# Kernel tuning notes

Measured on AMD Instinct MI355X. Metric: run time of the kernel, lower is better.

Reference implementation:

```python
import jax, jax.numpy as jnp
import numpy as np

N, E = 50000, 400000
IN, HID, HEADS, OUT, EDIM = 128, 16, 8, 128, 32


def _lin(key, fan_in, fan_out, bias=True):
    k1, k2 = jax.random.split(key)
    s = 1.0 / np.sqrt(fan_in)
    W = jax.random.uniform(k1, (fan_in, fan_out), jnp.float32, -s, s)
    if bias:
        b = jax.random.uniform(k2, (fan_out,), jnp.float32, -s, s)
        return W, b
    return W


def setup_inputs() -> dict:
    key = jax.random.key(0)
    ks = jax.random.split(key, 16)
    x = jax.random.normal(ks[0], (N, IN), jnp.float32)
    edge_index = jax.random.randint(ks[1], (2, E), 0, N, jnp.int64)
    edge_feats = jax.random.normal(ks[2], (E, EDIM), jnp.float32)
    H1 = HEADS * HID  # 128
    Wq1, bq1 = _lin(ks[3], IN, H1)
    Wk1, bk1 = _lin(ks[4], IN, H1)
    Wv1, bv1 = _lin(ks[5], IN, H1)
    We1 = _lin(ks[6], EDIM, H1, bias=False)
    Ws1, bs1 = _lin(ks[7], IN, H1)
    Wq2, bq2 = _lin(ks[8], H1, OUT)
    Wk2, bk2 = _lin(ks[9], H1, OUT)
    Wv2, bv2 = _lin(ks[10], H1, OUT)
    We2 = _lin(ks[11], EDIM, OUT, bias=False)
    Ws2, bs2 = _lin(ks[12], H1, OUT)
    return dict(x=x, edge_index=edge_index, edge_feats=edge_feats,
                Wq1=Wq1, bq1=bq1, Wk1=Wk1, bk1=bk1, Wv1=Wv1, bv1=bv1, We1=We1, Ws1=Ws1, bs1=bs1,
                Wq2=Wq2, bq2=bq2, Wk2=Wk2, bk2=bk2, Wv2=Wv2, bv2=bv2, We2=We2, Ws2=Ws2, bs2=bs2)


def transformer_conv(x, src, dst, e, Wq, bq, Wk, bk, Wv, bv, We, Ws, bs, heads, ch, concat):
    # PyG TransformerConv: project at nodes, gather to edges.
    n = x.shape[0]
    q = (x @ Wq + bq).reshape(n, heads, ch)[dst]          # [E,H,C]
    k = (x @ Wk + bk).reshape(n, heads, ch)[src]
    v = (x @ Wv + bv).reshape(n, heads, ch)[src]
    ee = (e @ We).reshape(-1, heads, ch)                   # edge conditioning
    k = k + ee
    v = v + ee
    alpha = (q * k).sum(-1) / jnp.sqrt(jnp.asarray(ch, x.dtype))  # [E,H]
    # per-destination segment softmax
    m = jax.ops.segment_max(alpha, dst, num_segments=n)
    m = jnp.where(jnp.isfinite(m), m, 0.0)
    ea = jnp.exp(alpha - m[dst])
    denom = jax.ops.segment_sum(ea, dst, num_segments=n)
    attn = ea / jnp.maximum(denom[dst], 1e-16)
    out = jax.ops.segment_sum(attn[:, :, None] * v, dst, num_segments=n)  # [N,H,C]
    out = out.reshape(n, heads * ch) if concat else out.mean(axis=1)
    return out + x @ Ws + bs  # root_weight skip


def reference(x, edge_index, edge_feats,
              Wq1, bq1, Wk1, bk1, Wv1, bv1, We1, Ws1, bs1,
              Wq2, bq2, Wk2, bk2, Wv2, bv2, We2, Ws2, bs2):
    src, dst = edge_index[0], edge_index[1]
    h = jax.nn.relu(transformer_conv(x, src, dst, edge_feats,
                                     Wq1, bq1, Wk1, bk1, Wv1, bv1, We1, Ws1, bs1,
                                     HEADS, HID, True))
    # dropout p=0.0 (eval) -> identity
    out = jax.nn.relu(transformer_conv(h, src, dst, edge_feats,
                                       Wq2, bq2, Wk2, bk2, Wv2, bv2, We2, Ws2, bs2,
                                       1, OUT, False))
    return out
```

## Files before the change

kernel.cpp:

```cpp
#include <hip/hip_runtime.h>


using u16 = unsigned short;
using u32 = unsigned int;

#define NODES 50000
#define EDGES 400000
#define NB196 196

typedef __attribute__((ext_vector_type(8))) short bf16x8;
typedef __attribute__((ext_vector_type(4))) float f32x4;

__device__ __forceinline__ float bflo(u32 u) { return __uint_as_float(u << 16); }
__device__ __forceinline__ float bfhi(u32 u) { return __uint_as_float(u & 0xffff0000u); }
__device__ __forceinline__ u16 f2bf(float f) {
    u32 u = __float_as_uint(f);
    u += 0x7fffu + ((u >> 16) & 1u);
    return (u16)(u >> 16);
}
__device__ __forceinline__ u32 pack2(float a, float b) {
    return (u32)f2bf(a) | ((u32)f2bf(b) << 16);
}

template <int CTRL>
__device__ __forceinline__ float dpp_addf(float x) {
    int y = __builtin_amdgcn_update_dpp(0, __float_as_int(x), CTRL, 0xF, 0xF, true);
    return x + __int_as_float(y);
}
template <int GRP>
__device__ __forceinline__ float grp_sum(float p, int lane) {
    p = dpp_addf<0xB1>(p);
    p = dpp_addf<0x4E>(p);
    p = dpp_addf<0x141>(p);
    if (GRP == 64) {
        p = dpp_addf<0x140>(p);
        p += __int_as_float(__builtin_amdgcn_ds_swizzle(__float_as_int(p), 0x401F));
        p += __int_as_float(__builtin_amdgcn_ds_bpermute((lane ^ 32) << 2,
                                                         __float_as_int(p)));
    }
    return p;
}

__global__ __launch_bounds__(256) void fill_sentinel(float* __restrict__ out, int n, float val) {
    int i = blockIdx.x * 256 + threadIdx.x;
    if (i < n) out[i] = val;
}

__global__ __launch_bounds__(64) void detect_fmt(const u32* __restrict__ xw,
                                                 const int* __restrict__ eraw,
                                                 int* __restrict__ flags) {
    int lane = threadIdx.x;
    u32 e = (xw[lane] >> 7) & 0xffu;
    unsigned long long sane = __ballot(e >= 90u && e <= 141u);
    unsigned long long zodd = __ballot(eraw[1 + 2 * lane] == 0);
    if (lane == 0) {
        flags[0] = (sane == ~0ull) ? 0 : 1;
        flags[1] = (zodd == ~0ull) ? 1 : 0;
    }
}

__global__ __launch_bounds__(256) void convert_x(const void* __restrict__ X,
                                                 const int* __restrict__ flags,
                                                 u16* __restrict__ xbf, int total) {
    int i = (blockIdx.x * 256 + threadIdx.x) * 8;
    if (i >= total) return;
    if (flags[0]) {
        const float* xf = (const float*)X + i;
        float4 lo = *reinterpret_cast<const float4*>(xf);
        float4 hi = *reinterpret_cast<const float4*>(xf + 4);
        uint4 val = make_uint4(pack2(lo.x, lo.y), pack2(lo.z, lo.w),
                               pack2(hi.x, hi.y), pack2(hi.z, hi.w));
        *reinterpret_cast<uint4*>(xbf + i) = val;
    } else {
        *reinterpret_cast<uint4*>(xbf + i) =
            *reinterpret_cast<const uint4*>((const u16*)X + i);
    }
}

struct TPtrs {
    const void* src[10];
    u16*        dst[10];
    int         K[10];
};

__global__ __launch_bounds__(256) void transpose_w(TPtrs P, const int* __restrict__ fmt) {
    int m = blockIdx.x;
    int f = *fmt;
    int K = P.K[m];
    int quarter = (K * 128) >> 2;
    u16* d = P.dst[m];
    int base = blockIdx.y * quarter;
    const float* sf = (const float*)P.src[m];
    const u16*   sb = (const u16*)P.src[m];
    for (int idx = base + threadIdx.x; idx < base + quarter; idx += 256) {
        int k = idx >> 7, n = idx & 127;
        d[n * K + k] = f ? f2bf(sf[idx]) : sb[idx];
    }
}

__global__ __launch_bounds__(256) void count_deg(const int* __restrict__ raw,
                                                 const int* __restrict__ flags,
                                                 int* __restrict__ deg, int E) {
    int e = blockIdx.x * 256 + threadIdx.x;
    if (e < E) {
        int f = flags[1];
        int d = f ? raw[2 * (E + e)] : raw[E + e];
        if ((unsigned)d < (unsigned)NODES) atomicAdd(&deg[d], 1);
    }
}

__device__ __forceinline__ int block_scan256(int v) {
    __shared__ int ws[4];
    int t = threadIdx.x, lane = t & 63, w = t >> 6;
    int x = v;
#pragma unroll
    for (int off = 1; off < 64; off <<= 1) {
        int y = __shfl_up(x, off, 64);
        if (lane >= off) x += y;
    }
    if (lane == 63) ws[w] = x;
    __syncthreads();
#pragma unroll
    for (int j = 0; j < 3; ++j)
        if (j < w) x += ws[j];
    return x;
}

__global__ __launch_bounds__(256) void scan_a(const int* __restrict__ deg,
                                              int* __restrict__ bsum, int n) {
    int i = blockIdx.x * 256 + threadIdx.x;
    int v = (i < n) ? deg[i] : 0;
    int incl = block_scan256(v);
    if (threadIdx.x == 255) bsum[blockIdx.x] = incl;
}

__global__ __launch_bounds__(256) void scan_b(int* __restrict__ bsum, int nb) {
    int t = threadIdx.x;
    int v = (t < nb) ? bsum[t] : 0;
    int incl = block_scan256(v);
    if (t < nb) bsum[t] = incl - v;
}

__global__ __launch_bounds__(256) void scan_c(const int* __restrict__ deg,
                                              const int* __restrict__ bsum,
                                              int* __restrict__ row_ptr,
                                              int* __restrict__ cursor, int n) {
    int b = blockIdx.x;
    int i = b * 256 + threadIdx.x;
    int v = (i < n) ? deg[i] : 0;
    int incl = block_scan256(v) + bsum[b];
    if (i < n) {
        row_ptr[i + 1] = incl;
        cursor[i] = incl - v;
    }
    if (i == 0) row_ptr[0] = 0;
}

__global__ __launch_bounds__(256) void fill_csr(const int* __restrict__ raw,
                                                const int* __restrict__ flags,
                                                int* __restrict__ cursor,
                                                int* __restrict__ srcs,
                                                int* __restrict__ eids, int E) {
    int e = blockIdx.x * 256 + threadIdx.x;
    if (e < E) {
        int f = flags[1];
        int d = f ? raw[2 * (E + e)] : raw[E + e];
        int s = f ? raw[2 * e] : raw[e];
        if ((unsigned)d < (unsigned)NODES && (unsigned)s < (unsigned)NODES) {
            int pos = atomicAdd(&cursor[d], 1);
            if ((unsigned)pos < (unsigned)E) { srcs[pos] = s; eids[pos] = e; }
        }
    }
}

__global__ __launch_bounds__(256) void gemm128(
    const u16* __restrict__ A, const int* __restrict__ flags,
    const u16* __restrict__ Wt0, const u16* __restrict__ Wt1,
    const u16* __restrict__ Wt2, const u16* __restrict__ Wt3,
    const void* __restrict__ b0, const void* __restrict__ b1,
    const void* __restrict__ b2, const void* __restrict__ b3,
    u16* __restrict__ O0, u16* __restrict__ O1,
    u16* __restrict__ O2, u16* __restrict__ O3,
    int M) {
    constexpr int K = 128;
    constexpr int PAD = K + 8;
    constexpr int KV = K / 8;
    __shared__ u16 Asl[64 * PAD];
    __shared__ u16 Bsl[128 * PAD];

    int f = flags[0];
    const u16* Wt; const void* bias; u16* O;
    switch (blockIdx.y) {
        case 0: Wt = Wt0; bias = b0; O = O0; break;
        case 1: Wt = Wt1; bias = b1; O = O1; break;
        case 2: Wt = Wt2; bias = b2; O = O2; break;
        default: Wt = Wt3; bias = b3; O = O3; break;
    }
    int m0 = blockIdx.x * 64;

    for (int idx = threadIdx.x; idx < 64 * KV; idx += 256) {
        int r = idx / KV, cv = idx % KV;
        int gr = m0 + r;
        uint4 val = make_uint4(0, 0, 0, 0);
        if (gr < M) val = *reinterpret_cast<const uint4*>(A + (size_t)gr * K + cv * 8);
        *reinterpret_cast<uint4*>(&Asl[r * PAD + cv * 8]) = val;
    }
    for (int idx = threadIdx.x; idx < 128 * KV; idx += 256) {
        int r = idx / KV, cv = idx % KV;
        *reinterpret_cast<uint4*>(&Bsl[r * PAD + cv * 8]) =
            *reinterpret_cast<const uint4*>(Wt + r * K + cv * 8);
    }
    __syncthreads();

    int lane = threadIdx.x & 63, wv = threadIdx.x >> 6;
    int l15 = lane & 15;
    int quad = lane >> 4;
    int kq = quad * 8;

    f32x4 b4[8];
#pragma unroll
    for (int nt = 0; nt < 8; ++nt) {
        int col0 = nt * 16 + quad * 4;
        if (bias) {
            if (f) {
                b4[nt] = *reinterpret_cast<const f32x4*>((const float*)bias + col0);
            } else {
                uint2 bu = *reinterpret_cast<const uint2*>((const u16*)bias + col0);
                b4[nt][0] = bflo(bu.x); b4[nt][1] = bfhi(bu.x);
                b4[nt][2] = bflo(bu.y); b4[nt][3] = bfhi(bu.y);
            }
        } else {
            b4[nt][0] = b4[nt][1] = b4[nt][2] = b4[nt][3] = 0.f;
        }
    }

    f32x4 acc[8] = {};
#pragma unroll
    for (int k0 = 0; k0 < K; k0 += 32) {
        bf16x8 xf = *reinterpret_cast<const bf16x8*>(&Asl[(wv * 16 + l15) * PAD + k0 + kq]);
#pragma unroll
        for (int nt = 0; nt < 8; ++nt) {
            bf16x8 wf = *reinterpret_cast<const bf16x8*>(&Bsl[(nt * 16 + l15) * PAD + k0 + kq]);
            acc[nt] = __builtin_amdgcn_mfma_f32_16x16x32_bf16(wf, xf, acc[nt], 0, 0, 0);
        }
    }

    int row = m0 + wv * 16 + l15;
    if (row < M) {
        u16* Orow = O + (size_t)row * 128;
#pragma unroll
        for (int nt = 0; nt < 8; ++nt) {
            uint2 pk;
            pk.x = pack2(acc[nt][0] + b4[nt][0], acc[nt][1] + b4[nt][1]);
            pk.y = pack2(acc[nt][2] + b4[nt][2], acc[nt][3] + b4[nt][3]);
            *reinterpret_cast<uint2*>(Orow + nt * 16 + quad * 4) = pk;
        }
    }
}

__global__ __launch_bounds__(256) void gemm_ee(
    const int* __restrict__ eids, const void* __restrict__ EF,
    const u16* __restrict__ WtE1 , const u16* __restrict__ WtE2,
    const int* __restrict__ flags,
    u16* __restrict__ EE1, u16* __restrict__ EE2, int Etot) {
    constexpr int PAD = 40;
    __shared__ u16 Asl[64 * PAD];
    __shared__ u16 Bsl[2][128 * PAD];
    int p0 = blockIdx.x * 64;
    int f = flags[0];
    bool dual = (EE2 != nullptr);

    {
        int r = threadIdx.x >> 2, seg = threadIdx.x & 3;
        int p = p0 + r;
        int e = (p < Etot) ? eids[p] : 0;
        uint4 val;
        if (f) {
            const float* src = (const float*)EF + (size_t)e * 32 + seg * 8;
            float4 lo = *reinterpret_cast<const float4*>(src);
            float4 hi = *reinterpret_cast<const float4*>(src + 4);
            val = make_uint4(pack2(lo.x, lo.y), pack2(lo.z, lo.w),
                             pack2(hi.x, hi.y), pack2(hi.z, hi.w));
        } else {
            val = *reinterpret_cast<const uint4*>((const u16*)EF + (size_t)e * 32 + seg * 8);
        }
        *reinterpret_cast<uint4*>(&Asl[r * PAD + seg * 8]) = val;
    }
    for (int idx = threadIdx.x; idx < 128 * 4; idx += 256) {
        int r = idx >> 2, seg = idx & 3;
        *reinterpret_cast<uint4*>(&Bsl[0][r * PAD + seg * 8]) =
            *reinterpret_cast<const uint4*>(WtE1 + r * 32 + seg * 8);
    }
    if (dual) {
        for (int idx = threadIdx.x; idx < 128 * 4; idx += 256) {
            int r = idx >> 2, seg = idx & 3;
            *reinterpret_cast<uint4*>(&Bsl[1][r * PAD + seg * 8]) =
                *reinterpret_cast<const uint4*>(WtE2 + r * 32 + seg * 8);
        }
    }
    __syncthreads();

    int lane = threadIdx.x & 63, wv = threadIdx.x >> 6;
    int l15 = lane & 15;
    int quad = lane >> 4;
    int kq = quad * 8;
    int pos = p0 + wv * 16 + l15;
    bool ok = pos < Etot;
    bf16x8 ef8 = *reinterpret_cast<const bf16x8*>(&Asl[(wv * 16 + l15) * PAD + kq]);

    {
        f32x4 acc[8] = {};
#pragma unroll
        for (int nt = 0; nt < 8; ++nt) {
            bf16x8 wf = *reinterpret_cast<const bf16x8*>(&Bsl[0][(nt * 16 + l15) * PAD + kq]);
            acc[nt] = __builtin_amdgcn_mfma_f32_16x16x32_bf16(wf, ef8, acc[nt], 0, 0, 0);
        }
        if (ok) {
            u16* Orow = EE1 + (size_t)pos * 128;
#pragma unroll
            for (int nt = 0; nt < 8; ++nt) {
                uint2 pk;
                pk.x = pack2(acc[nt][0], acc[nt][1]);
                pk.y = pack2(acc[nt][2], acc[nt][3]);
                *reinterpret_cast<uint2*>(Orow + nt * 16 + quad * 4) = pk;
            }
        }
    }
    if (dual) {
        f32x4 acc[8] = {};
#pragma unroll
        for (int nt = 0; nt < 8; ++nt) {
            bf16x8 wf = *reinterpret_cast<const bf16x8*>(&Bsl[1][(nt * 16 + l15) * PAD + kq]);
            acc[nt] = __builtin_amdgcn_mfma_f32_16x16x32_bf16(wf, ef8, acc[nt], 0, 0, 0);
        }
        if (ok) {
            u16* Orow = EE2 + (size_t)pos * 128;
#pragma unroll
            for (int nt = 0; nt < 8; ++nt) {
                uint2 pk;
                pk.x = pack2(acc[nt][0], acc[nt][1]);
                pk.y = pack2(acc[nt][2], acc[nt][3]);
                *reinterpret_cast<uint2*>(Orow + nt * 16 + quad * 4) = pk;
            }
        }
    }
}

template <int HEADS, int F32OUT>
__global__ __launch_bounds__(256) void attn_kernel(
    const int* __restrict__ row_ptr, const int* __restrict__ srcs,
    const u16* __restrict__ Q, const u16* __restrict__ Kn,
    const u16* __restrict__ Vn, const u16* __restrict__ EE,
    const u16* __restrict__ SK, void* __restrict__ OUT, int nn) {
    int wv = threadIdx.x >> 6, lane = threadIdx.x & 63;
    int node = blockIdx.x * 4 + wv;
    if (node >= nn) return;
    int c0 = lane * 2;

    u32 qb = *reinterpret_cast<const u32*>(Q + (size_t)node * 128 + c0);
    float q0 = bflo(qb), q1 = bfhi(qb);

    int beg = row_ptr[node], end = row_ptr[node + 1];
    const float scale = (HEADS == 8) ? 0.25f : 0.08838834764831845f;
    constexpr int GRP = (HEADS == 8) ? 8 : 64;

    float l_run = 0.f, a0 = 0.f, a1 = 0.f;

    auto edge_step = [&](u32 kbv, u32 vbv, u32 ebv) {
        float e0 = bflo(ebv), e1 = bfhi(ebv);
        float k0 = bflo(kbv) + e0, k1 = bfhi(kbv) + e1;
        float p = q0 * k0 + q1 * k1;
        p = grp_sum<GRP>(p, lane);
        float w = __expf(p * scale);
        l_run += w;
        a0 = fmaf(w, bflo(vbv) + e0, a0);
        a1 = fmaf(w, bfhi(vbv) + e1, a1);
    };

    int i = beg;
    for (; i + 8 <= end; i += 8) {
        int sA[8];
#pragma unroll
        for (int j = 0; j < 8; ++j) sA[j] = srcs[i + j];
        u32 kb[8], vb[8], eb[8];
#pragma unroll
        for (int j = 0; j < 8; ++j) {
            kb[j] = *reinterpret_cast<const u32*>(Kn + (size_t)sA[j] * 128 + c0);
            vb[j] = *reinterpret_cast<const u32*>(Vn + (size_t)sA[j] * 128 + c0);
            eb[j] = *reinterpret_cast<const u32*>(EE + (size_t)(i + j) * 128 + c0);
        }
#pragma unroll
        for (int j = 0; j < 8; ++j) edge_step(kb[j], vb[j], eb[j]);
    }
    for (; i < end; ++i) {
        int s = srcs[i];
        u32 kbv = *reinterpret_cast<const u32*>(Kn + (size_t)s * 128 + c0);
        u32 vbv = *reinterpret_cast<const u32*>(Vn + (size_t)s * 128 + c0);
        u32 ebv = *reinterpret_cast<const u32*>(EE + (size_t)i * 128 + c0);
        edge_step(kbv, vbv, ebv);
    }

    float inv = 1.f / fmaxf(l_run, 1e-16f);
    u32 sb = *reinterpret_cast<const u32*>(SK + (size_t)node * 128 + c0);
    float o0 = fmaxf(a0 * inv + bflo(sb), 0.f);
    float o1 = fmaxf(a1 * inv + bfhi(sb), 0.f);
    if (F32OUT) {
        *reinterpret_cast<float2*>((float*)OUT + (size_t)node * 128 + c0) = make_float2(o0, o1);
    } else {
        *reinterpret_cast<u32*>((u16*)OUT + (size_t)node * 128 + c0) = pack2(o0, o1);
    }
}

template <int HEADS, int F32OUT>
__global__ __launch_bounds__(256) void attn_fused(
    const int* __restrict__ row_ptr, const int* __restrict__ srcs,
    const int* __restrict__ eids, const int* __restrict__ flags,
    const u16* __restrict__ Q, const u16* __restrict__ Kn,
    const u16* __restrict__ Vn, const void* __restrict__ EF,
    const void* __restrict__ We, const u16* __restrict__ SK,
    void* __restrict__ OUT, int nn) {
    int wv = threadIdx.x >> 6, lane = threadIdx.x & 63;
    int node = blockIdx.x * 4 + wv;
    if (node >= nn) return;
    int c0 = lane * 2;
    int f = flags[0];

    float wf0[32], wf1[32];
    if (f) {
        const float* Wef = (const float*)We;
#pragma unroll
        for (int d = 0; d < 32; ++d) {
            float2 w2 = *reinterpret_cast<const float2*>(Wef + d * 128 + c0);
            wf0[d] = w2.x; wf1[d] = w2.y;
        }
    } else {
        const u16* Web = (const u16*)We;
#pragma unroll
        for (int d = 0; d < 32; ++d) {
            u32 w = *reinterpret_cast<const u32*>(Web + d * 128 + c0);
            wf0[d] = bflo(w); wf1[d] = bfhi(w);
        }
    }

    u32 qb = *reinterpret_cast<const u32*>(Q + (size_t)node * 128 + c0);
    float q0 = bflo(qb), q1 = bfhi(qb);
    int beg = row_ptr[node], end = row_ptr[node + 1];
    const float scale = (HEADS == 8) ? 0.25f : 0.08838834764831845f;
    constexpr int GRP = (HEADS == 8) ? 8 : 64;
    float l_run = 0.f, a0 = 0.f, a1 = 0.f;

    for (int i = beg; i < end; ++i) {
        int s = srcs[i], e = eids[i];
        u32 kbv = *reinterpret_cast<const u32*>(Kn + (size_t)s * 128 + c0);
        u32 vbv = *reinterpret_cast<const u32*>(Vn + (size_t)s * 128 + c0);
        float efv[32];
        if (f) {
            const float* eff = (const float*)EF + (size_t)e * 32;
#pragma unroll
            for (int t = 0; t < 8; ++t) {
                float4 q4 = *reinterpret_cast<const float4*>(eff + t * 4);
                efv[4 * t] = q4.x; efv[4 * t + 1] = q4.y;
                efv[4 * t + 2] = q4.z; efv[4 * t + 3] = q4.w;
            }
        } else {
            const uint4* efp = reinterpret_cast<const uint4*>((const u16*)EF + (size_t)e * 32);
            uint4 ea = efp[0], eb2 = efp[1], ec = efp[2], ed = efp[3];
            u32 efw[16] = {ea.x, ea.y, ea.z, ea.w, eb2.x, eb2.y, eb2.z, eb2.w,
                           ec.x, ec.y, ec.z, ec.w, ed.x, ed.y, ed.z, ed.w};
#pragma unroll
            for (int t = 0; t < 16; ++t) {
                efv[2 * t] = bflo(efw[t]);
                efv[2 * t + 1] = bfhi(efw[t]);
            }
        }
        float ee0 = 0.f, ee1 = 0.f;
#pragma unroll
        for (int t = 0; t < 32; ++t) {
            ee0 = fmaf(efv[t], wf0[t], ee0);
            ee1 = fmaf(efv[t], wf1[t], ee1);
        }
        float k0 = bflo(kbv) + ee0, k1 = bfhi(kbv) + ee1;
        float p = q0 * k0 + q1 * k1;
        p = grp_sum<GRP>(p, lane);
        float w = __expf(p * scale);
        l_run += w;
        a0 = fmaf(w, bflo(vbv) + ee0, a0);
        a1 = fmaf(w, bfhi(vbv) + ee1, a1);
    }

    float inv = 1.f / fmaxf(l_run, 1e-16f);
    u32 sb = *reinterpret_cast<const u32*>(SK + (size_t)node * 128 + c0);
    float o0 = fmaxf(a0 * inv + bflo(sb), 0.f);
    float o1 = fmaxf(a1 * inv + bfhi(sb), 0.f);
    if (F32OUT) {
        *reinterpret_cast<float2*>((float*)OUT + (size_t)node * 128 + c0) = make_float2(o0, o1);
    } else {
        *reinterpret_cast<u32*>((u16*)OUT + (size_t)node * 128 + c0) = pack2(o0, o1);
    }
}

extern "C" void kernel_launch(void* const* d_in, const int* in_sizes, int n_in,
                              void* d_out, int out_size, void* d_ws, size_t ws_size,
                              hipStream_t stream) {
    const int N = NODES, E = EDGES;
    const void* x  = d_in[0];
    const int*  ei = (const int*)d_in[1];
    const void* ef = d_in[2];
    const void* Wq1 = d_in[3];  const void* bq1 = d_in[4];
    const void* Wk1 = d_in[5];  const void* bk1 = d_in[6];
    const void* Wv1 = d_in[7];  const void* bv1 = d_in[8];
    const void* We1 = d_in[9];
    const void* Ws1 = d_in[10]; const void* bs1 = d_in[11];
    const void* Wq2 = d_in[12]; const void* bq2 = d_in[13];
    const void* Wk2 = d_in[14]; const void* bk2 = d_in[15];
    const void* Wv2 = d_in[16]; const void* bv2 = d_in[17];
    const void* We2 = d_in[18];
    const void* Ws2 = d_in[19]; const void* bs2 = d_in[20];

    char* ws = (char*)d_ws;
    size_t off = 0;
    auto carve = [&](size_t bytes) -> void* {
        void* p = ws + off;
        off += (bytes + 255) & ~(size_t)255;
        return p;
    };

    u16* WtQ1 = (u16*)carve(128 * 128 * 2);
    u16* WtK1 = (u16*)carve(128 * 128 * 2);
    u16* WtV1 = (u16*)carve(128 * 128 * 2);
    u16* WtS1 = (u16*)carve(128 * 128 * 2);
    u16* WtQ2 = (u16*)carve(128 * 128 * 2);
    u16* WtK2 = (u16*)carve(128 * 128 * 2);
    u16* WtV2 = (u16*)carve(128 * 128 * 2);
    u16* WtS2 = (u16*)carve(128 * 128 * 2);
    u16* WtE1 = (u16*)carve(128 * 32 * 2);
    u16* WtE2 = (u16*)carve(128 * 32 * 2);
    int* flags   = (int*)carve(256);
    int* deg     = (int*)carve((size_t)N * 4);
    int* bsum    = (int*)carve((size_t)NB196 * 4);
    int* row_ptr = (int*)carve((size_t)(N + 1) * 4);
    int* cursor  = (int*)carve((size_t)N * 4);
    int* srcs    = (int*)carve((size_t)E * 4);
    int* eids    = (int*)carve((size_t)E * 4);
    u16* xbf = (u16*)carve((size_t)N * 128 * 2);
    u16* q  = (u16*)carve((size_t)N * 128 * 2);
    u16* k  = (u16*)carve((size_t)N * 128 * 2);
    u16* v  = (u16*)carve((size_t)N * 128 * 2);
    u16* sk = (u16*)carve((size_t)N * 128 * 2);
    u16* h  = (u16*)carve((size_t)N * 128 * 2);
    const size_t REQ_BASE = off;
    u16* ee1 = (u16*)carve((size_t)E * 128 * 2);
    const size_t REQ_BIG = off;
    u16* ee2 = (u16*)carve((size_t)E * 128 * 2);
    const size_t REQ_2EE = off;
    const bool DUAL  = (ws_size >= REQ_2EE);
    const bool MATOK = (ws_size >= REQ_BIG);

    if (ws_size < REQ_BASE) {
        hipLaunchKernelGGL(fill_sentinel, dim3((out_size + 255) / 256), dim3(256), 0, stream,
                           (float*)d_out, out_size, 16.0f * (float)(ws_size >> 20));
        return;
    }

    hipLaunchKernelGGL(detect_fmt, dim3(1), dim3(64), 0, stream, (const u32*)x, ei, flags);

    hipLaunchKernelGGL(convert_x, dim3((N * 128 / 8 + 255) / 256), dim3(256), 0, stream,
                       x, flags, xbf, N * 128);

    TPtrs tp;
    tp.src[0] = Wq1; tp.dst[0] = WtQ1; tp.K[0] = 128;
    tp.src[1] = Wk1; tp.dst[1] = WtK1; tp.K[1] = 128;
    tp.src[2] = Wv1; tp.dst[2] = WtV1; tp.K[2] = 128;
    tp.src[3] = Ws1; tp.dst[3] = WtS1; tp.K[3] = 128;
    tp.src[4] = Wq2; tp.dst[4] = WtQ2; tp.K[4] = 128;
    tp.src[5] = Wk2; tp.dst[5] = WtK2; tp.K[5] = 128;
    tp.src[6] = Wv2; tp.dst[6] = WtV2; tp.K[6] = 128;
    tp.src[7] = Ws2; tp.dst[7] = WtS2; tp.K[7] = 128;
    tp.src[8] = We1; tp.dst[8] = WtE1; tp.K[8] = 32;
    tp.src[9] = We2; tp.dst[9] = WtE2; tp.K[9] = 32;
    hipLaunchKernelGGL(transpose_w, dim3(10, 4), dim3(256), 0, stream, tp, flags);

    (void)hipMemsetAsync(deg, 0, (size_t)N * 4, stream);
    hipLaunchKernelGGL(count_deg, dim3((E + 255) / 256), dim3(256), 0, stream, ei, flags, deg, E);
    hipLaunchKernelGGL(scan_a, dim3(NB196), dim3(256), 0, stream, deg, bsum, N);
    hipLaunchKernelGGL(scan_b, dim3(1), dim3(256), 0, stream, bsum, NB196);
    hipLaunchKernelGGL(scan_c, dim3(NB196), dim3(256), 0, stream, deg, bsum, row_ptr, cursor, N);
    hipLaunchKernelGGL(fill_csr, dim3((E + 255) / 256), dim3(256), 0, stream, ei, flags, cursor,
                       srcs, eids, E);

    const int gN = (N + 63) / 64;
    const int gE = E / 64;
    const int gA = (N + 3) / 4;

    if (MATOK) {
        hipLaunchKernelGGL(gemm_ee, dim3(gE), dim3(256), 0, stream,
                           eids, ef, WtE1, WtE2, flags,
                           ee1, DUAL ? ee2 : (u16*)nullptr, E);
    }

    hipLaunchKernelGGL(gemm128, dim3(gN, 4), dim3(256), 0, stream,
                       xbf, flags, WtQ1, WtK1, WtV1, WtS1,
                       bq1, bk1, bv1, bs1, q, k, v, sk, N);
    if (MATOK) {
        hipLaunchKernelGGL((attn_kernel<8, 0>), dim3(gA), dim3(256), 0, stream,
                           row_ptr, srcs, q, k, v, ee1, sk, (void*)h, N);
    } else {
        hipLaunchKernelGGL((attn_fused<8, 0>), dim3(gA), dim3(256), 0, stream,
                           row_ptr, srcs, eids, flags, q, k, v, ef, We1, sk, (void*)h, N);
    }

    hipLaunchKernelGGL(gemm128, dim3(gN, 4), dim3(256), 0, stream,
                       h, flags, WtQ2, WtK2, WtV2, WtS2,
                       bq2, bk2, bv2, bs2, q, k, v, sk, N);
    if (MATOK) {
        if (!DUAL) {
            hipLaunchKernelGGL(gemm_ee, dim3(gE), dim3(256), 0, stream,
                               eids, ef, WtE2, (const u16*)nullptr, flags,
                               ee1, (u16*)nullptr, E);
        }
        hipLaunchKernelGGL((attn_kernel<1, 1>), dim3(gA), dim3(256), 0, stream,
                           row_ptr, srcs, q, k, v, DUAL ? ee2 : ee1, sk, d_out, N);
    } else {
        hipLaunchKernelGGL((attn_fused<1, 1>), dim3(gA), dim3(256), 0, stream,
                           row_ptr, srcs, eids, flags, q, k, v, ef, We2, sk, d_out, N);
    }
}
```

Baseline: 456.8 us.

## Fold edge projection into query and aggregate raw edge features instead of materializing EE

Instead of materializing per-edge projected edge embeddings (E x 128 bf16 per layer), the query is pre-multiplied by We per head (q·We computed at node level via extra GEMM columns). Raw 32-dim edge features are gathered once in CSR order and dotted against it. The value-side edge term is accumulated as a weighted sum of raw edge features and projected through We once per node at the end. This removes the large EE write/read traffic per edge in exchange for extra node GEMM outputs, a per-node 32x128 epilogue, and some extra bf16 rounding of the folded weights.

```diff
diff --git a/kernel.cpp b/kernel.cpp
--- a/kernel.cpp
+++ b/kernel.cpp
@@ -20,6 +20,10 @@
 }
 __device__ __forceinline__ u32 pack2(float a, float b) {
     return (u32)f2bf(a) | ((u32)f2bf(b) << 16);
+}
+__device__ __forceinline__ float rdv(const void* p, int i, int f) {
+    return f ? ((const float*)p)[i]
+             : __uint_as_float(((u32) reinterpret_cast<const u16*>(p)[i]) << 16);
 }
 
 template <int CTRL>
@@ -78,9 +82,9 @@
 }
 
 struct TPtrs {
-    const void* src[10];
-    u16*        dst[10];
-    int         K[10];
+    const void* src[8];
+    u16*        dst[8];
+    int         K[8];
 };
 
 __global__ __launch_bounds__(256) void transpose_w(TPtrs P, const int* __restrict__ fmt) {
@@ -95,6 +99,51 @@
     for (int idx = base + threadIdx.x; idx < base + quarter; idx += 256) {
         int k = idx >> 7, n = idx & 127;
         d[n * K + k] = f ? f2bf(sf[idx]) : sb[idx];
+    }
+}
+
+struct WqeP {
+    const void *Wq1, *We1, *bq1, *Wq2, *We2, *bq2;
+    u16 *WtA, *WtB, *Wt2;
+    float *bqe1, *bqe2;
+};
+
+__global__ __launch_bounds__(256) void make_wqe(WqeP P, const int* __restrict__ flags) {
+    int f = flags[0];
+    int idx = blockIdx.x * 256 + threadIdx.x;
+    if (idx < 32768) {
+        int col = idx >> 7, i = idx & 127;
+        int hh = col >> 5, d = col & 31;
+        float s = 0.f;
+#pragma unroll
+        for (int c = 0; c < 16; ++c)
+            s += rdv(P.Wq1, i * 128 + hh * 16 + c, f) * rdv(P.We1, d * 128 + hh * 16 + c, f);
+        if (col < 128) P.WtA[col * 128 + i] = f2bf(s);
+        else           P.WtB[(col - 128) * 128 + i] = f2bf(s);
+    } else if (idx < 49152) {
+        int t = idx - 32768;
+        int col = t >> 7, i = t & 127;
+        float s = 0.f;
+        if (col < 32) {
+            for (int c = 0; c < 128; ++c)
+                s += rdv(P.Wq2, i * 128 + c, f) * rdv(P.We2, col * 128 + c, f);
+        }
+        P.Wt2[col * 128 + i] = f2bf(s);
+    } else if (idx < 49408) {
+        int col = idx - 49152;
+        int hh = col >> 5, d = col & 31;
+        float s = 0.f;
+#pragma unroll
+        for (int c = 0; c < 16; ++c)
+            s += rdv(P.bq1, hh * 16 + c, f) * rdv(P.We1, d * 128 + hh * 16 + c, f);
+        P.bqe1[col] = s;
+    } else if (idx < 49536) {
+        int d = idx - 49408;
+        float s = 0.f;
+        if (d < 32)
+            for (int c = 0; c < 128; ++c)
+                s += rdv(P.bq2, c, f) * rdv(P.We2, d * 128 + c, f);
+        P.bqe2[d] = s;
     }
 }
 
@@ -173,29 +222,46 @@
     }
 }
 
+__global__ __launch_bounds__(256) void gather_ef(const int* __restrict__ eids,
+                                                 const void* __restrict__ EF,
+                                                 const int* __restrict__ flags,
+                                                 u16* __restrict__ EFG, int E) {
+    int t = blockIdx.x * 256 + threadIdx.x;
+    int pos = t >> 2, seg = t & 3;
+    if (pos >= E) return;
+    int e = eids[pos];
+    uint4 val;
+    if (flags[0]) {
+        const float* src = (const float*)EF + (size_t)e * 32 + seg * 8;
+        float4 lo = *reinterpret_cast<const float4*>(src);
+        float4 hi = *reinterpret_cast<const float4*>(src + 4);
+        val = make_uint4(pack2(lo.x, lo.y), pack2(lo.z, lo.w),
+                         pack2(hi.x, hi.y), pack2(hi.z, hi.w));
+    } else {
+        val = *reinterpret_cast<const uint4*>((const u16*)EF + (size_t)e * 32 + seg * 8);
+    }
+    *reinterpret_cast<uint4*>(EFG + (size_t)pos * 32 + seg * 8) = val;
+}
+
+struct GemmSets {
+    const u16*  Wt[6];
+    const void* bias[6];
+    u16*        O[6];
+    int         bf32[6];
+};
+
 __global__ __launch_bounds__(256) void gemm128(
-    const u16* __restrict__ A, const int* __restrict__ flags,
-    const u16* __restrict__ Wt0, const u16* __restrict__ Wt1,
-    const u16* __restrict__ Wt2, const u16* __restrict__ Wt3,
-    const void* __restrict__ b0, const void* __restrict__ b1,
-    const void* __restrict__ b2, const void* __restrict__ b3,
-    u16* __restrict__ O0, u16* __restrict__ O1,
-    u16* __restrict__ O2, u16* __restrict__ O3,
-    int M) {
+    const u16* __restrict__ A, const int* __restrict__ flags, GemmSets S, int M) {
     constexpr int K = 128;
     constexpr int PAD = K + 8;
     constexpr int KV = K / 8;
     __shared__ u16 Asl[64 * PAD];
     __shared__ u16 Bsl[128 * PAD];
 
-    int f = flags[0];
-    const u16* Wt; const void* bias; u16* O;
-    switch (blockIdx.y) {
-        case 0: Wt = Wt0; bias = b0; O = O0; break;
-        case 1: Wt = Wt1; bias = b1; O = O1; break;
-        case 2: Wt = Wt2; bias = b2; O = O2; break;
-        default: Wt = Wt3; bias = b3; O = O3; break;
-    }
+    const u16*  Wt   = S.Wt[blockIdx.y];
+    const void* bias = S.bias[blockIdx.y];
+    u16*        O    = S.O[blockIdx.y];
+    int f = S.bf32[blockIdx.y] ? 1 : flags[0];
     int m0 = blockIdx.x * 64;
 
     for (int idx = threadIdx.x; idx < 64 * KV; idx += 256) {
@@ -258,240 +324,110 @@
     }
 }
 
-__global__ __launch_bounds__(256) void gemm_ee(
-    const int* __restrict__ eids, const void* __restrict__ EF,
-    const u16* __restrict__ WtE1 , const u16* __restrict__ WtE2,
-    const int* __restrict__ flags,
-    u16* __restrict__ EE1, u16* __restrict__ EE2, int Etot) {
-    constexpr int PAD = 40;
-    __shared__ u16 Asl[64 * PAD];
-    __shared__ u16 Bsl[2][128 * PAD];
-    int p0 = blockIdx.x * 64;
-    int f = flags[0];
-    bool dual = (EE2 != nullptr);
-
-    {
-        int r = threadIdx.x >> 2, seg = threadIdx.x & 3;
-        int p = p0 + r;
-        int e = (p < Etot) ? eids[p] : 0;
-        uint4 val;
-        if (f) {
-            const float* src = (const float*)EF + (size_t)e * 32 + seg * 8;
-            float4 lo = *reinterpret_cast<const float4*>(src);
-            float4 hi = *reinterpret_cast<const float4*>(src + 4);
-            val = make_uint4(pack2(lo.x, lo.y), pack2(lo.z, lo.w),
-                             pack2(hi.x, hi.y), pack2(hi.z, hi.w));
-        } else {
-            val = *reinterpret_cast<const uint4*>((const u16*)EF + (size_t)e * 32 + seg * 8);
-        }
-        *reinterpret_cast<uint4*>(&Asl[r * PAD + seg * 8]) = val;
-    }
-    for (int idx = threadIdx.x; idx < 128 * 4; idx += 256) {
-        int r = idx >> 2, seg = idx & 3;
-        *reinterpret_cast<uint4*>(&Bsl[0][r * PAD + seg * 8]) =
-            *reinterpret_cast<const uint4*>(WtE1 + r * 32 + seg * 8);
-    }
-    if (dual) {
-        for (int idx = threadIdx.x; idx < 128 * 4; idx += 256) {
-            int r = idx >> 2, seg = idx & 3;
-            *reinterpret_cast<uint4*>(&Bsl[1][r * PAD + seg * 8]) =
-                *reinterpret_cast<const uint4*>(WtE2 + r * 32 + seg * 8);
-        }
-    }
-    __syncthreads();
-
-    int lane = threadIdx.x & 63, wv = threadIdx.x >> 6;
-    int l15 = lane & 15;
-    int quad = lane >> 4;
-    int kq = quad * 8;
-    int pos = p0 + wv * 16 + l15;
-    bool ok = pos < Etot;
-    bf16x8 ef8 = *reinterpret_cast<const bf16x8*>(&Asl[(wv * 16 + l15) * PAD + kq]);
-
-    {
-        f32x4 acc[8] = {};
-#pragma unroll
-        for (int nt = 0; nt < 8; ++nt) {
-            bf16x8 wf = *reinterpret_cast<const bf16x8*>(&Bsl[0][(nt * 16 + l15) * PAD + kq]);
-            acc[nt] = __builtin_amdgcn_mfma_f32_16x16x32_bf16(wf, ef8, acc[nt], 0, 0, 0);
-        }
-        if (ok) {
-            u16* Orow = EE1 + (size_t)pos * 128;
-#pragma unroll
-            for (int nt = 0; nt < 8; ++nt) {
-                uint2 pk;
-                pk.x = pack2(acc[nt][0], acc[nt][1]);
-                pk.y = pack2(acc[nt][2], acc[nt][3]);
-                *reinterpret_cast<uint2*>(Orow + nt * 16 + quad * 4) = pk;
-            }
-        }
-    }
-    if (dual) {
-        f32x4 acc[8] = {};
-#pragma unroll
-        for (int nt = 0; nt < 8; ++nt) {
-            bf16x8 wf = *reinterpret_cast<const bf16x8*>(&Bsl[1][(nt * 16 + l15) * PAD + kq]);
-            acc[nt] = __builtin_amdgcn_mfma_f32_16x16x32_bf16(wf, ef8, acc[nt], 0, 0, 0);
-        }
-        if (ok) {
-            u16* Orow = EE2 + (size_t)pos * 128;
-#pragma unroll
-            for (int nt = 0; nt < 8; ++nt) {
-                uint2 pk;
-                pk.x = pack2(acc[nt][0], acc[nt][1]);
-                pk.y = pack2(acc[nt][2], acc[nt][3]);
-                *reinterpret_cast<uint2*>(Orow + nt * 16 + quad * 4) = pk;
-            }
-        }
-    }
-}
-
 template <int HEADS, int F32OUT>
 __global__ __launch_bounds__(256) void attn_kernel(
     const int* __restrict__ row_ptr, const int* __restrict__ srcs,
     const u16* __restrict__ Q, const u16* __restrict__ Kn,
-    const u16* __restrict__ Vn, const u16* __restrict__ EE,
-    const u16* __restrict__ SK, void* __restrict__ OUT, int nn) {
+    const u16* __restrict__ Vn, const u16* __restrict__ EFG,
+    const u16* __restrict__ QWA, const u16* __restrict__ QWB,
+    const u16* __restrict__ SK, const void* __restrict__ We,
+    const int* __restrict__ flags, void* __restrict__ OUT, int nn) {
+    __shared__ u32 WeLds[32 * 64];
+    __shared__ float Flds[4][8][36];
+
+    int fmt = flags[0];
+    for (int t = threadIdx.x; t < 2048; t += 256) {
+        int d = t >> 6, l = t & 63;
+        u32 val;
+        if (fmt) {
+            const float* wp = (const float*)We + d * 128 + 2 * l;
+            val = pack2(wp[0], wp[1]);
+        } else {
+            val = *reinterpret_cast<const u32*>((const u16*)We + d * 128 + 2 * l);
+        }
+        WeLds[t] = val;
+    }
+    __syncthreads();
+
     int wv = threadIdx.x >> 6, lane = threadIdx.x & 63;
     int node = blockIdx.x * 4 + wv;
     if (node >= nn) return;
+    int h = lane >> 3, j = lane & 7;
     int c0 = lane * 2;
 
+    const float scale = (HEADS == 8) ? 0.25f : 0.08838834764831845f;
+    const float escale = (HEADS == 8) ? scale : scale * 0.125f;
+    constexpr int GRP = (HEADS == 8) ? 8 : 64;
+
     u32 qb = *reinterpret_cast<const u32*>(Q + (size_t)node * 128 + c0);
-    float q0 = bflo(qb), q1 = bfhi(qb);
+    float q0 = bflo(qb) * scale, q1 = bfhi(qb) * scale;
+
+    const u16* qp = (HEADS == 8)
+        ? ((h < 4 ? QWA : QWB) + (size_t)node * 128 + (h & 3) * 32 + j * 4)
+        : (QWA + (size_t)node * 128 + j * 4);
+    uint2 qwu = *reinterpret_cast<const uint2*>(qp);
+    float qw0 = bflo(qwu.x) * escale, qw1 = bfhi(qwu.x) * escale;
+    float qw2 = bflo(qwu.y) * escale, qw3 = bfhi(qwu.y) * escale;
 
     int beg = row_ptr[node], end = row_ptr[node + 1];
-    const float scale = (HEADS == 8) ? 0.25f : 0.08838834764831845f;
-    constexpr int GRP = (HEADS == 8) ? 8 : 64;
-
     float l_run = 0.f, a0 = 0.f, a1 = 0.f;
-
-    auto edge_step = [&](u32 kbv, u32 vbv, u32 ebv) {
-        float e0 = bflo(ebv), e1 = bfhi(ebv);
-        float k0 = bflo(kbv) + e0, k1 = bfhi(kbv) + e1;
-        float p = q0 * k0 + q1 * k1;
+    float f0 = 0.f, f1 = 0.f, f2 = 0.f, f3 = 0.f;
+
+    const u16* efp = EFG + j * 4;
+
+    auto edge_step = [&](u32 kbv, u32 vbv, uint2 ebv) {
+        float e0 = bflo(ebv.x), e1 = bfhi(ebv.x);
+        float e2 = bflo(ebv.y), e3 = bfhi(ebv.y);
+        float p = q0 * bflo(kbv);
+        p = fmaf(q1, bfhi(kbv), p);
+        p = fmaf(qw0, e0, p); p = fmaf(qw1, e1, p);
+        p = fmaf(qw2, e2, p); p = fmaf(qw3, e3, p);
         p = grp_sum<GRP>(p, lane);
-        float w = __expf(p * scale);
+        float w = __expf(p);
         l_run += w;
-        a0 = fmaf(w, bflo(vbv) + e0, a0);
-        a1 = fmaf(w, bfhi(vbv) + e1, a1);
+        a0 = fmaf(w, bflo(vbv), a0);
+        a1 = fmaf(w, bfhi(vbv), a1);
+        f0 = fmaf(w, e0, f0); f1 = fmaf(w, e1, f1);
+        f2 = fmaf(w, e2, f2); f3 = fmaf(w, e3, f3);
     };
 
     int i = beg;
     for (; i + 8 <= end; i += 8) {
         int sA[8];
 #pragma unroll
-        for (int j = 0; j < 8; ++j) sA[j] = srcs[i + j];
-        u32 kb[8], vb[8], eb[8];
-#pragma unroll
-        for (int j = 0; j < 8; ++j) {
-            kb[j] = *reinterpret_cast<const u32*>(Kn + (size_t)sA[j] * 128 + c0);
-            vb[j] = *reinterpret_cast<const u32*>(Vn + (size_t)sA[j] * 128 + c0);
-            eb[j] = *reinterpret_cast<const u32*>(EE + (size_t)(i + j) * 128 + c0);
-        }
-#pragma unroll
-        for (int j = 0; j < 8; ++j) edge_step(kb[j], vb[j], eb[j]);
+        for (int t = 0; t < 8; ++t) sA[t] = srcs[i + t];
+        u32 kb[8], vb[8]; uint2 eb[8];
+#pragma unroll
+        for (int t = 0; t < 8; ++t) {
+            kb[t] = *reinterpret_cast<const u32*>(Kn + (size_t)sA[t] * 128 + c0);
+            vb[t] = *reinterpret_cast<const u32*>(Vn + (size_t)sA[t] * 128 + c0);
+            eb[t] = *reinterpret_cast<const uint2*>(efp + (size_t)(i + t) * 32);
+        }
+#pragma unroll
+        for (int t = 0; t < 8; ++t) edge_step(kb[t], vb[t], eb[t]);
     }
     for (; i < end; ++i) {
         int s = srcs[i];
         u32 kbv = *reinterpret_cast<const u32*>(Kn + (size_t)s * 128 + c0);
         u32 vbv = *reinterpret_cast<const u32*>(Vn + (size_t)s * 128 + c0);
-        u32 ebv = *reinterpret_cast<const u32*>(EE + (size_t)i * 128 + c0);
+        uint2 ebv = *reinterpret_cast<const uint2*>(efp + (size_t)i * 32);
         edge_step(kbv, vbv, ebv);
+    }
+
+    *reinterpret_cast<float4*>(&Flds[wv][h][4 * j]) = make_float4(f0, f1, f2, f3);
+    float acc0 = 0.f, acc1 = 0.f;
+#pragma unroll
+    for (int d = 0; d < 32; ++d) {
+        float Fd = Flds[wv][h][d];
+        u32 we = WeLds[d * 64 + lane];
+        acc0 = fmaf(Fd, bflo(we), acc0);
+        acc1 = fmaf(Fd, bfhi(we), acc1);
     }
 
     float inv = 1.f / fmaxf(l_run, 1e-16f);
     u32 sb = *reinterpret_cast<const u32*>(SK + (size_t)node * 128 + c0);
-    float o0 = fmaxf(a0 * inv + bflo(sb), 0.f);
-    float o1 = fmaxf(a1 * inv + bfhi(sb), 0.f);
-    if (F32OUT) {
-        *reinterpret_cast<float2*>((float*)OUT + (size_t)node * 128 + c0) = make_float2(o0, o1);
-    } else {
-        *reinterpret_cast<u32*>((u16*)OUT + (size_t)node * 128 + c0) = pack2(o0, o1);
-    }
-}
-
-template <int HEADS, int F32OUT>
-__global__ __launch_bounds__(256) void attn_fused(
-    const int* __restrict__ row_ptr, const int* __restrict__ srcs,
-    const int* __restrict__ eids, const int* __restrict__ flags,
-    const u16* __restrict__ Q, const u16* __restrict__ Kn,
-    const u16* __restrict__ Vn, const void* __restrict__ EF,
-    const void* __restrict__ We, const u16* __restrict__ SK,
-    void* __restrict__ OUT, int nn) {
-    int wv = threadIdx.x >> 6, lane = threadIdx.x & 63;
-    int node = blockIdx.x * 4 + wv;
-    if (node >= nn) return;
-    int c0 = lane * 2;
-    int f = flags[0];
-
-    float wf0[32], wf1[32];
-    if (f) {
-        const float* Wef = (const float*)We;
-#pragma unroll
-        for (int d = 0; d < 32; ++d) {
-            float2 w2 = *reinterpret_cast<const float2*>(Wef + d * 128 + c0);
-            wf0[d] = w2.x; wf1[d] = w2.y;
-        }
-    } else {
-        const u16* Web = (const u16*)We;
-#pragma unroll
-        for (int d = 0; d < 32; ++d) {
-            u32 w = *reinterpret_cast<const u32*>(Web + d * 128 + c0);
-            wf0[d] = bflo(w); wf1[d] = bfhi(w);
-        }
-    }
-
-    u32 qb = *reinterpret_cast<const u32*>(Q + (size_t)node * 128 + c0);
-    float q0 = bflo(qb), q1 = bfhi(qb);
-    int beg = row_ptr[node], end = row_ptr[node + 1];
-    const float scale = (HEADS == 8) ? 0.25f : 0.08838834764831845f;
-    constexpr int GRP = (HEADS == 8) ? 8 : 64;
-    float l_run = 0.f, a0 = 0.f, a1 = 0.f;
-
-    for (int i = beg; i < end; ++i) {
-        int s = srcs[i], e = eids[i];
-        u32 kbv = *reinterpret_cast<const u32*>(Kn + (size_t)s * 128 + c0);
-        u32 vbv = *reinterpret_cast<const u32*>(Vn + (size_t)s * 128 + c0);
-        float efv[32];
-        if (f) {
-            const float* eff = (const float*)EF + (size_t)e * 32;
-#pragma unroll
-            for (int t = 0; t < 8; ++t) {
-                float4 q4 = *reinterpret_cast<const float4*>(eff + t * 4);
-                efv[4 * t] = q4.x; efv[4 * t + 1] = q4.y;
-                efv[4 * t + 2] = q4.z; efv[4 * t + 3] = q4.w;
-            }
-        } else {
-            const uint4* efp = reinterpret_cast<const uint4*>((const u16*)EF + (size_t)e * 32);
-            uint4 ea = efp[0], eb2 = efp[1], ec = efp[2], ed = efp[3];
-            u32 efw[16] = {ea.x, ea.y, ea.z, ea.w, eb2.x, eb2.y, eb2.z, eb2.w,
-                           ec.x, ec.y, ec.z, ec.w, ed.x, ed.y, ed.z, ed.w};
-#pragma unroll
-            for (int t = 0; t < 16; ++t) {
-                efv[2 * t] = bflo(efw[t]);
-                efv[2 * t + 1] = bfhi(efw[t]);
-            }
-        }
-        float ee0 = 0.f, ee1 = 0.f;
-#pragma unroll
-        for (int t = 0; t < 32; ++t) {
-            ee0 = fmaf(efv[t], wf0[t], ee0);
-            ee1 = fmaf(efv[t], wf1[t], ee1);
-        }
-        float k0 = bflo(kbv) + ee0, k1 = bfhi(kbv) + ee1;
-        float p = q0 * k0 + q1 * k1;
-        p = grp_sum<GRP>(p, lane);
-        float w = __expf(p * scale);
-        l_run += w;
-        a0 = fmaf(w, bflo(vbv) + ee0, a0);
-        a1 = fmaf(w, bfhi(vbv) + ee1, a1);
-    }
-
-    float inv = 1.f / fmaxf(l_run, 1e-16f);
-    u32 sb = *reinterpret_cast<const u32*>(SK + (size_t)node * 128 + c0);
-    float o0 = fmaxf(a0 * inv + bflo(sb), 0.f);
-    float o1 = fmaxf(a1 * inv + bfhi(sb), 0.f);
+    float o0 = fmaxf(fmaf(a0 + acc0, inv, bflo(sb)), 0.f);
+    float o1 = fmaxf(fmaf(a1 + acc1, inv, bfhi(sb)), 0.f);
     if (F32OUT) {
         *reinterpret_cast<float2*>((float*)OUT + (size_t)node * 128 + c0) = make_float2(o0, o1);
     } else {
@@ -533,8 +469,11 @@
     u16* WtK2 = (u16*)carve(128 * 128 * 2);
     u16* WtV2 = (u16*)carve(128 * 128 * 2);
     u16* WtS2 = (u16*)carve(128 * 128 * 2);
-    u16* WtE1 = (u16*)carve(128 * 32 * 2);
-    u16* WtE2 = (u16*)carve(128 * 32 * 2);
+    u16* WtqA = (u16*)carve(128 * 128 * 2);
+    u16* WtqB = (u16*)carve(128 * 128 * 2);
+    u16* Wtq2 = (u16*)carve(128 * 128 * 2);
+    float* bqe1 = (float*)carve(256 * 4);
+    float* bqe2 = (float*)carve(128 * 4);
     int* flags   = (int*)carve(256);
     int* deg     = (int*)carve((size_t)N * 4);
     int* bsum    = (int*)carve((size_t)NB196 * 4);
@@ -542,21 +481,19 @@
     int* cursor  = (int*)carve((size_t)N * 4);
     int* srcs    = (int*)carve((size_t)E * 4);
     int* eids    = (int*)carve((size_t)E * 4);
-    u16* xbf = (u16*)carve((size_t)N * 128 * 2);
-    u16* q  = (u16*)carve((size_t)N * 128 * 2);
-    u16* k  = (u16*)carve((size_t)N * 128 * 2);
-    u16* v  = (u16*)carve((size_t)N * 128 * 2);
-    u16* sk = (u16*)carve((size_t)N * 128 * 2);
-    u16* h  = (u16*)carve((size_t)N * 128 * 2);
-    const size_t REQ_BASE = off;
-    u16* ee1 = (u16*)carve((size_t)E * 128 * 2);
-    const size_t REQ_BIG = off;
-    u16* ee2 = (u16*)carve((size_t)E * 128 * 2);
-    const size_t REQ_2EE = off;
-    const bool DUAL  = (ws_size >= REQ_2EE);
-    const bool MATOK = (ws_size >= REQ_BIG);
-
-    if (ws_size < REQ_BASE) {
+    u16* xbf  = (u16*)carve((size_t)N * 128 * 2);
+    u16* q    = (u16*)carve((size_t)N * 128 * 2);
+    u16* k    = (u16*)carve((size_t)N * 128 * 2);
+    u16* v    = (u16*)carve((size_t)N * 128 * 2);
+    u16* sk   = (u16*)carve((size_t)N * 128 * 2);
+    u16* h    = (u16*)carve((size_t)N * 128 * 2);
+    u16* qweA = (u16*)carve((size_t)N * 128 * 2);
+    u16* qweB = (u16*)carve((size_t)N * 128 * 2);
+    u16* qwe2 = (u16*)carve((size_t)N * 128 * 2);
+    u16* efg  = (u16*)carve((size_t)E * 32 * 2);
+    const size_t REQ = off;
+
+    if (ws_size < REQ) {
         hipLaunchKernelGGL(fill_sentinel, dim3((out_size + 255) / 256), dim3(256), 0, stream,
                            (float*)d_out, out_size, 16.0f * (float)(ws_size >> 20));
         return;
@@ -576,9 +513,14 @@
     tp.src[5] = Wk2; tp.dst[5] = WtK2; tp.K[5] = 128;
     tp.src[6] = Wv2; tp.dst[6] = WtV2; tp.K[6] = 128;
     tp.src[7] = Ws2; tp.dst[7] = WtS2; tp.K[7] = 128;
-    tp.src[8] = We1; tp.dst[8] = WtE1; tp.K[8] = 32;
-    tp.src[9] = We2; tp.dst[9] = WtE2; tp.K[9] = 32;
-    hipLaunchKernelGGL(transpose_w, dim3(10, 4), dim3(256), 0, stream, tp, flags);
+    hipLaunchKernelGGL(transpose_w, dim3(8, 4), dim3(256), 0, stream, tp, flags);
+
+    WqeP wp;
+    wp.Wq1 = Wq1; wp.We1 = We1; wp.bq1 = bq1;
+    wp.Wq2 = Wq2; wp.We2 = We2; wp.bq2 = bq2;
+    wp.WtA = WtqA; wp.WtB = WtqB; wp.Wt2 = Wtq2;
+    wp.bqe1 = bqe1; wp.bqe2 = bqe2;
+    hipLaunchKernelGGL(make_wqe, dim3(194), dim3(256), 0, stream, wp, flags);
 
     (void)hipMemsetAsync(deg, 0, (size_t)N * 4, stream);
     hipLaunchKernelGGL(count_deg, dim3((E + 255) / 256), dim3(256), 0, stream, ei, flags, deg, E);
@@ -588,40 +530,35 @@
     hipLaunchKernelGGL(fill_csr, dim3((E + 255) / 256), dim3(256), 0, stream, ei, flags, cursor,
                        srcs, eids, E);
 
+    hipLaunchKernelGGL(gather_ef, dim3(E * 4 / 256), dim3(256), 0, stream,
+                       eids, ef, flags, efg, E);
+
     const int gN = (N + 63) / 64;
-    const int gE = E / 64;
     const int gA = (N + 3) / 4;
 
-    if (MATOK) {
-        hipLaunchKernelGGL(gemm_ee, dim3(gE), dim3(256), 0, stream,
-                           eids, ef, WtE1, WtE2, flags,
-                           ee1, DUAL ? ee2 : (u16*)nullptr, E);
-    }
-
-    hipLaunchKernelGGL(gemm128, dim3(gN, 4), dim3(256), 0, stream,
-                       xbf, flags, WtQ1, WtK1, WtV1, WtS1,
-                       bq1, bk1, bv1, bs1, q, k, v, sk, N);
-    if (MATOK) {
-        hipLaunchKernelGGL((attn_kernel<8, 0>), dim3(gA), dim3(256), 0, stream,
-                           row_ptr, srcs, q, k, v, ee1, sk, (void*)h, N);
-    } else {
-        hipLaunchKernelGGL((attn_fused<8, 0>), dim3(gA), dim3(256), 0, stream,
-                           row_ptr, srcs, eids, flags, q, k, v, ef, We1, sk, (void*)h, N);
-    }
-
-    hipLaunchKernelGGL(gemm128, dim3(gN, 4), dim3(256), 0, stream,
-                       h, flags, WtQ2, WtK2, WtV2, WtS2,
-                       bq2, bk2, bv2, bs2, q, k, v, sk, N);
-    if (MATOK) {
-        if (!DUAL) {
-            hipLaunchKernelGGL(gemm_ee, dim3(gE), dim3(256), 0, stream,
-                               eids, ef, WtE2, (const u16*)nullptr, flags,
-                               ee1, (u16*)nullptr, E);
-        }
-        hipLaunchKernelGGL((attn_kernel<1, 1>), dim3(gA), dim3(256), 0, stream,
-                           row_ptr, srcs, q, k, v, DUAL ? ee2 : ee1, sk, d_out, N);
-    } else {
-        hipLaunchKernelGGL((attn_fused<1, 1>), dim3(gA), dim3(256), 0, stream,
-                           row_ptr, srcs, eids, flags, q, k, v, ef, We2, sk, d_out, N);
-    }
-}
+    {
+        GemmSets S;
+        S.Wt[0] = WtQ1; S.bias[0] = bq1;  S.O[0] = q;    S.bf32[0] = 0;
+        S.Wt[1] = WtK1; S.bias[1] = bk1;  S.O[1] = k;    S.bf32[1] = 0;
+        S.Wt[2] = WtV1; S.bias[2] = bv1;  S.O[2] = v;    S.bf32[2] = 0;
+        S.Wt[3] = WtS1; S.bias[3] = bs1;  S.O[3] = sk;   S.bf32[3] = 0;
+        S.Wt[4] = WtqA; S.bias[4] = bqe1;       S.O[4] = qweA; S.bf32[4] = 1;
+        S.Wt[5] = WtqB; S.bias[5] = bqe1 + 128; S.O[5] = qweB; S.bf32[5] = 1;
+        hipLaunchKernelGGL(gemm128, dim3(gN, 6), dim3(256), 0, stream, xbf, flags, S, N);
+    }
+    hipLaunchKernelGGL((attn_kernel<8, 0>), dim3(gA), dim3(256), 0, stream,
+                       row_ptr, srcs, q, k, v, efg, qweA, qweB, sk, We1, flags, (void*)h, N);
+
+    {
+        GemmSets S;
+        S.Wt[0] = WtQ2; S.bias[0] = bq2;  S.O[0] = q;    S.bf32[0] = 0;
+        S.Wt[1] = WtK2; S.bias[1] = bk2;  S.O[1] = k;    S.bf32[1] = 0;
+        S.Wt[2] = WtV2; S.bias[2] = bv2;  S.O[2] = v;    S.bf32[2] = 0;
+        S.Wt[3] = WtS2; S.bias[3] = bs2;  S.O[3] = sk;   S.bf32[3] = 0;
+        S.Wt[4] = Wtq2; S.bias[4] = bqe2; S.O[4] = qwe2; S.bf32[4] = 1;
+        S.Wt[5] = Wtq2; S.bias[5] = bqe2; S.O[5] = qwe2; S.bf32[5] = 1;
+        hipLaunchKernelGGL(gemm128, dim3(gN, 5), dim3(256), 0, stream, h, flags, S, N);
+    }
+    hipLaunchKernelGGL((attn_kernel<1, 1>), dim3(gA), dim3(256), 0, stream,
+                       row_ptr, srcs, q, k, v, efg, qwe2, qwe2, sk, We2, flags, d_out, N);
+}
```

Result: slower. 546.6 us (+19.7%).
